# Performance work log

Hardware: AMD Instinct MI355X
Metric: run time of the kernel (lower is better)

Reference implementation:

```python
import jax, jax.numpy as jnp
import numpy as np

B, A, F = 8192, 8, 256      # batch, n_agents, per-agent obs feature dim
NA = 16                     # n_actions per agent
H1, H2 = 1024, 1024
OBS_D = A * F               # 2048 flattened obs dim
ACT_D = A * NA              # 128 joint action dim
IN_D = OBS_D + ACT_D        # 2176 MLP input dim


def setup_inputs() -> dict:
    key = jax.random.key(0)
    ks = jax.random.split(key, 8)
    s = 0.02
    return {
        "obs": jax.random.normal(ks[0], (B, A, F), dtype=jnp.float32),
        "all_actions": jax.random.uniform(ks[1], (B, ACT_D), dtype=jnp.float32),
        # per-agent stacked MLP params (agent axis first)
        "W1": jax.random.normal(ks[2], (A, IN_D, H1), dtype=jnp.float32) * s,
        "b1": jnp.zeros((A, H1), dtype=jnp.float32),
        "W2": jax.random.normal(ks[3], (A, H1, H2), dtype=jnp.float32) * s,
        "b2": jnp.zeros((A, H2), dtype=jnp.float32),
        "W3": jax.random.normal(ks[4], (A, H2, NA), dtype=jnp.float32) * s,
        "b3": jnp.zeros((A, NA), dtype=jnp.float32),
    }


def reference(obs, all_actions, W1, b1, W2, b2, W3, b3):
    b_s = obs.shape[0]
    obs_flat = obs.reshape(b_s, OBS_D)                      # [B, A*F]
    # mask[a, g] = 0 on agent a's own action block, 1 elsewhere
    mask = 1.0 - jnp.repeat(jnp.eye(A, dtype=obs.dtype), NA, axis=1)  # [A, A*NA]
    # split W1 into obs / action columns (equivalent to concat-then-dense)
    W1o = W1[:, :OBS_D, :]                                  # [A, OBS_D, H1]
    W1a = W1[:, OBS_D:, :]                                  # [A, ACT_D, H1]
    h1 = jax.nn.relu(
        jnp.einsum("bd,adh->bah", obs_flat, W1o)
        + jnp.einsum("bg,ag,agh->bah", all_actions, mask, W1a)
        + b1
    )                                                        # [B, A, H1]
    h2 = jax.nn.relu(jnp.einsum("bah,ahk->bak", h1, W2) + b2)  # [B, A, H2]
    out = jnp.einsum("bak,akn->ban", h2, W3) + b3              # [B, A, NA]
    return out.reshape(b_s, A * NA)
```

## Files before the change

kernel.cpp:

```cpp
#include <hip/hip_runtime.h>
#include <hip/hip_bf16.h>
#include <cstdint>
#include <cstddef>

typedef __bf16 bf16;
typedef __attribute__((ext_vector_type(8))) __bf16 bf16x8;
typedef __attribute__((ext_vector_type(4))) float f32x4;
typedef __attribute__((ext_vector_type(4))) int i32x4;
typedef __attribute__((address_space(3))) const bf16* lds_cp;

#define B_SZ  8192
#define NAGENT 8
#define NA_N  16
#define OBS_DD 2048
#define ACT_DD 128
#define IN_DD 2176
#define H1_D  1024
#define H2_D  1024

#define BM 256
#define BN 256
#define BK 64
#define GRID_M (B_SZ / BM)
#define GRID_N (1024 / BN)

__device__ __forceinline__ void gload16(const void* g, void* l) {
    __builtin_amdgcn_global_load_lds(
        (__attribute__((address_space(1))) void*)(g),
        (__attribute__((address_space(3))) void*)(l), 16, 0, 0);
}


__global__ void k_convert_x(const float* __restrict__ obs,
                            const float* __restrict__ act,
                            bf16* __restrict__ xb) {
    const int chunks = IN_DD / 8;
    int idx = blockIdx.x * blockDim.x + threadIdx.x;
    if (idx >= B_SZ * chunks) return;
    int b = idx / chunks;
    int c8 = idx - b * chunks;
    const float* src = (c8 < OBS_DD / 8)
        ? (obs + (size_t)b * OBS_DD + c8 * 8)
        : (act + (size_t)b * ACT_DD + (c8 - OBS_DD / 8) * 8);
    float4 v0 = ((const float4*)src)[0];
    float4 v1 = ((const float4*)src)[1];
    bf16x8 o;
    o[0] = (bf16)v0.x; o[1] = (bf16)v0.y; o[2] = (bf16)v0.z; o[3] = (bf16)v0.w;
    o[4] = (bf16)v1.x; o[5] = (bf16)v1.y; o[6] = (bf16)v1.z; o[7] = (bf16)v1.w;
    ((bf16x8*)(xb + (size_t)b * IN_DD))[c8] = o;
}

__global__ void k_transpose_w(const float* __restrict__ src, bf16* __restrict__ dst,
                              int K, int H, int maskStart) {
    __shared__ float tile[32][33];
    int a = blockIdx.z;
    int k0 = blockIdx.x * 32, h0 = blockIdx.y * 32;
    const float* s = src + (size_t)a * K * H;
    bf16* d = dst + (size_t)a * K * H;
    int tx = threadIdx.x, ty = threadIdx.y;
    #pragma unroll
    for (int i = 0; i < 32; i += 8) {
        int k = k0 + ty + i;
        float v = s[(size_t)k * H + h0 + tx];
        if (k >= maskStart) {
            int g = k - maskStart;
            if ((g >> 4) == a) v = 0.f;
        }
        tile[ty + i][tx] = v;
    }
    __syncthreads();
    #pragma unroll
    for (int i = 0; i < 32; i += 8) {
        d[(size_t)(h0 + ty + i) * K + k0 + tx] = (bf16)tile[tx][ty + i];
    }
}

__global__ void k_transpose_w3(const float* __restrict__ src, bf16* __restrict__ dst) {
    int idx = blockIdx.x * blockDim.x + threadIdx.x;
    if (idx >= NAGENT * NA_N * H2_D) return;
    int a = idx / (NA_N * H2_D);
    int n = (idx / H2_D) % NA_N;
    int k = idx % H2_D;
    dst[idx] = (bf16)src[(size_t)a * H2_D * NA_N + (size_t)k * NA_N + n];
}

__global__ void k_init_out(const float* __restrict__ b3, float* __restrict__ out) {
    int i = blockIdx.x * blockDim.x + threadIdx.x;
    if (i < B_SZ * NAGENT * NA_N) out[i] = b3[i & 127];
}

#define DSR4(d0, d1, d2, d3, addr, O0, O1, O2, O3)                      \
    asm volatile("ds_read_b128 %0, %4 offset:" #O0 "\n\t"               \
                 "ds_read_b128 %1, %4 offset:" #O1 "\n\t"               \
                 "ds_read_b128 %2, %4 offset:" #O2 "\n\t"               \
                 "ds_read_b128 %3, %4 offset:" #O3                      \
                 : "=&v"(d0), "=&v"(d1), "=&v"(d2), "=&v"(d3)           \
                 : "v"(addr))

#define BC(x) __builtin_bit_cast(bf16x8, x)

template<int FUSE>
__global__ __launch_bounds__(512, 1)
void k_gemm256(const bf16* __restrict__ Ain, size_t aStride, int lda,
               const bf16* __restrict__ Bw, const float* __restrict__ bias,
               bf16* __restrict__ Cout, size_t cStride, int K,
               int aOff, int gridZ,
               const bf16* __restrict__ W3Tp, float* __restrict__ outp) {
    extern __shared__ bf16 lds[];

    const int tid = threadIdx.x;
    const int w = tid >> 6;
    const int l = tid & 63;

    int flat = blockIdx.x + GRID_M * (blockIdx.y + GRID_N * blockIdx.z);
    int q8 = (GRID_M * GRID_N * gridZ) >> 3;
    int lin2 = (flat & 7) * q8 + (flat >> 3);
    const int mt = lin2 % GRID_M;
    int rest = lin2 / GRID_M;
    const int ntile = rest % GRID_N;
    const int az = rest / GRID_N;
    const int aw = az + aOff;

    const int rowBase = mt * BM;
    const int colBase = ntile * BN;
    const bf16* Aag = Ain + (size_t)az * aStride;
    const bf16* Bag = Bw + (size_t)aw * (size_t)1024 * K;

    const int wr = (w >> 2) * 128;
    const int wc = (w & 3) * 64;
    const int lr = l & 15;
    const int lq = l >> 4;

    const int rowA = (wr + lr) * BK;
    const int rowB = (wc + lr) * BK;
    const int ck0 = ((lq ^ (lr & 7)) * 8);
    const int ck1 = (((4 + lq) ^ (lr & 7)) * 8);

    const int sRow = w * 16 + (l >> 3);
    const int sCol = ((l & 7) ^ (l >> 3)) * 8;
    const bf16* pA0 = Aag + (size_t)(rowBase + sRow) * lda + sCol;
    const bf16* pA1 = Aag + (size_t)(rowBase + 128 + sRow) * lda + sCol;
    const bf16* pB0 = Bag + (size_t)(colBase + sRow) * K + sCol;
    const bf16* pB1 = Bag + (size_t)(colBase + 128 + sRow) * K + sCol;
    const size_t l8a = (size_t)8 * lda;
    const size_t l8b = (size_t)8 * K;

    const int nkt = K / BK;

#define STAGE_A(t1, half) do {                                              \
        const bf16* g_ = ((half) ? pA1 : pA0) + (t1) * BK;                  \
        bf16* d_ = &lds[(((t1) & 1) * 16384) + (half) * 8192 + w * 1024];   \
        gload16(g_, d_);                                                    \
        gload16(g_ + l8a, d_ + 512);                                        \
    } while (0)
#define STAGE_B(t2, half) do {                                              \
        const bf16* g_ = ((half) ? pB1 : pB0) + (t2) * BK;                  \
        bf16* d_ = &lds[32768 + (((t2) & 1) * 16384) + (half) * 8192 + w * 1024]; \
        gload16(g_, d_);                                                    \
        gload16(g_ + l8b, d_ + 512);                                        \
    } while (0)

    f32x4 acc[8][4] = {};
    i32x4 ra0, ra1, ra2, ra3;
    i32x4 rb0, rb1, rb2, rb3;
    i32x4 rc0, rc1, rc2, rc3;
    i32x4 rd0, rd1, rd2, rd3;
    i32x4 re0, re1, re2, re3;
    i32x4 rf0, rf1, rf2, rf3;

#define MFMA16(ACC0, A0, A1, A2, A3, B0, B1, B2, B3)                        \
    do {                                                                    \
        acc[ACC0+0][0] = __builtin_amdgcn_mfma_f32_16x16x32_bf16(BC(A0), BC(B0), acc[ACC0+0][0], 0, 0, 0); \
        acc[ACC0+1][0] = __builtin_amdgcn_mfma_f32_16x16x32_bf16(BC(A1), BC(B0), acc[ACC0+1][0], 0, 0, 0); \
        acc[ACC0+2][0] = __builtin_amdgcn_mfma_f32_16x16x32_bf16(BC(A2), BC(B0), acc[ACC0+2][0], 0, 0, 0); \
        acc[ACC0+3][0] = __builtin_amdgcn_mfma_f32_16x16x32_bf16(BC(A3), BC(B0), acc[ACC0+3][0], 0, 0, 0); \
        acc[ACC0+0][1] = __builtin_amdgcn_mfma_f32_16x16x32_bf16(BC(A0), BC(B1), acc[ACC0+0][1], 0, 0, 0); \
        acc[ACC0+1][1] = __builtin_amdgcn_mfma_f32_16x16x32_bf16(BC(A1), BC(B1), acc[ACC0+1][1], 0, 0, 0); \
        acc[ACC0+2][1] = __builtin_amdgcn_mfma_f32_16x16x32_bf16(BC(A2), BC(B1), acc[ACC0+2][1], 0, 0, 0); \
        acc[ACC0+3][1] = __builtin_amdgcn_mfma_f32_16x16x32_bf16(BC(A3), BC(B1), acc[ACC0+3][1], 0, 0, 0); \
        acc[ACC0+0][2] = __builtin_amdgcn_mfma_f32_16x16x32_bf16(BC(A0), BC(B2), acc[ACC0+0][2], 0, 0, 0); \
        acc[ACC0+1][2] = __builtin_amdgcn_mfma_f32_16x16x32_bf16(BC(A1), BC(B2), acc[ACC0+1][2], 0, 0, 0); \
        acc[ACC0+2][2] = __builtin_amdgcn_mfma_f32_16x16x32_bf16(BC(A2), BC(B2), acc[ACC0+2][2], 0, 0, 0); \
        acc[ACC0+3][2] = __builtin_amdgcn_mfma_f32_16x16x32_bf16(BC(A3), BC(B2), acc[ACC0+3][2], 0, 0, 0); \
        acc[ACC0+0][3] = __builtin_amdgcn_mfma_f32_16x16x32_bf16(BC(A0), BC(B3), acc[ACC0+0][3], 0, 0, 0); \
        acc[ACC0+1][3] = __builtin_amdgcn_mfma_f32_16x16x32_bf16(BC(A1), BC(B3), acc[ACC0+1][3], 0, 0, 0); \
        acc[ACC0+2][3] = __builtin_amdgcn_mfma_f32_16x16x32_bf16(BC(A2), BC(B3), acc[ACC0+2][3], 0, 0, 0); \
        acc[ACC0+3][3] = __builtin_amdgcn_mfma_f32_16x16x32_bf16(BC(A3), BC(B3), acc[ACC0+3][3], 0, 0, 0); \
    } while (0)

    STAGE_A(0, 0); STAGE_A(0, 1);
    STAGE_B(0, 0); STAGE_B(0, 1);
    asm volatile("s_waitcnt vmcnt(0)" ::: "memory");
    __builtin_amdgcn_s_barrier();

    for (int t = 0; t < nkt; ++t) {
        const int dbuf = (t & 1) * 16384;
        lds_cp adrA0 = (lds_cp)lds + (dbuf + rowA + ck0);
        lds_cp adrA1 = (lds_cp)lds + (dbuf + rowA + ck1);
        lds_cp adrB0 = (lds_cp)lds + (32768 + dbuf + rowB + ck0);
        lds_cp adrB1 = (lds_cp)lds + (32768 + dbuf + rowB + ck1);

        if (t + 1 < nkt) {
            STAGE_A(t + 1, 0); STAGE_A(t + 1, 1);
            STAGE_B(t + 1, 0); STAGE_B(t + 1, 1);
        }

        DSR4(ra0, ra1, ra2, ra3, adrA0, 0, 2048, 4096, 6144);
        DSR4(rb0, rb1, rb2, rb3, adrB0, 0, 2048, 4096, 6144);
        DSR4(rc0, rc1, rc2, rc3, adrA0, 8192, 10240, 12288, 14336);
        DSR4(rd0, rd1, rd2, rd3, adrB1, 0, 2048, 4096, 6144);

        asm volatile("s_waitcnt lgkmcnt(8)" ::: "memory");
        __builtin_amdgcn_sched_barrier(0);
        __builtin_amdgcn_s_setprio(1);
        MFMA16(0, ra0, ra1, ra2, ra3, rb0, rb1, rb2, rb3);
        __builtin_amdgcn_s_setprio(0);

        DSR4(re0, re1, re2, re3, adrA1, 0, 2048, 4096, 6144);
        asm volatile("s_waitcnt lgkmcnt(4)" ::: "memory");
        __builtin_amdgcn_sched_barrier(0);
        __builtin_amdgcn_s_setprio(1);
        MFMA16(4, rc0, rc1, rc2, rc3, rb0, rb1, rb2, rb3);
        __builtin_amdgcn_s_setprio(0);

        DSR4(rf0, rf1, rf2, rf3, adrA1, 8192, 10240, 12288, 14336);
        asm volatile("s_waitcnt lgkmcnt(4)" ::: "memory");
        __builtin_amdgcn_sched_barrier(0);
        __builtin_amdgcn_s_setprio(1);
        MFMA16(0, re0, re1, re2, re3, rd0, rd1, rd2, rd3);
        __builtin_amdgcn_s_setprio(0);

        asm volatile("s_waitcnt lgkmcnt(0)" ::: "memory");
        __builtin_amdgcn_sched_barrier(0);
        __builtin_amdgcn_s_setprio(1);
        MFMA16(4, rf0, rf1, rf2, rf3, rd0, rd1, rd2, rd3);
        __builtin_amdgcn_s_setprio(0);

        asm volatile("s_waitcnt vmcnt(0)" ::: "memory");
        __builtin_amdgcn_s_barrier();
    }
#undef STAGE_A
#undef STAGE_B
#undef MFMA16

    __syncthreads();
    const float* bAg = bias + (size_t)aw * 1024;
    float bb4[4];
    #pragma unroll
    for (int n = 0; n < 4; ++n) bb4[n] = bAg[colBase + wc + n * 16 + lr];
    #pragma unroll
    for (int m = 0; m < 8; ++m)
        #pragma unroll
        for (int n = 0; n < 4; ++n)
            #pragma unroll
            for (int r = 0; r < 4; ++r) {
                float v = acc[m][n][r] + bb4[n];
                v = fmaxf(v, 0.f);
                int row = wr + m * 16 + lq * 4 + r;
                int col = wc + n * 16 + lr;
                lds[row * 256 + ((((col >> 3) ^ (row & 7)) << 3) | (col & 7))] = (bf16)v;
            }
    __syncthreads();

    if constexpr (!FUSE) {
        bf16* Cg = Cout + (size_t)az * cStride + (size_t)rowBase * 1024 + colBase;
        const int er = tid >> 5;
        const int ec = tid & 31;
        #pragma unroll
        for (int i = 0; i < 16; ++i) {
            int row = i * 16 + er;
            int phys = ec ^ (row & 7);
            *(bf16x8*)&Cg[(size_t)row * 1024 + ec * 8] =
                *(const bf16x8*)&lds[row * 256 + phys * 8];
        }
    } else {
        const bf16* w3a = W3Tp + (size_t)aw * NA_N * H2_D;
        f32x4 oacc[2] = {};
        const int frow0 = w * 32;
        #pragma unroll
        for (int ks = 0; ks < 8; ++ks) {
            bf16x8 bfrag = *(const bf16x8*)&w3a[(size_t)lr * H2_D + colBase + ks * 32 + lq * 8];
            #pragma unroll
            for (int mm = 0; mm < 2; ++mm) {
                int row = frow0 + mm * 16 + lr;
                int lc = (ks * 4 + lq) ^ (row & 7);
                bf16x8 afrag = *(const bf16x8*)&lds[row * 256 + lc * 8];
                oacc[mm] = __builtin_amdgcn_mfma_f32_16x16x32_bf16(afrag, bfrag, oacc[mm], 0, 0, 0);
            }
        }
        #pragma unroll
        for (int mm = 0; mm < 2; ++mm)
            #pragma unroll
            for (int r = 0; r < 4; ++r)
                atomicAdd(&outp[(size_t)(rowBase + frow0 + mm * 16 + lq * 4 + r) * 128
                                + aw * NA_N + lr], oacc[mm][r]);
    }
}

extern "C" void kernel_launch(void* const* d_in, const int* in_sizes, int n_in,
                              void* d_out, int out_size, void* d_ws, size_t ws_size,
                              hipStream_t stream) {
    const float* obs = (const float*)d_in[0];
    const float* act = (const float*)d_in[1];
    const float* W1 = (const float*)d_in[2];
    const float* b1 = (const float*)d_in[3];
    const float* W2 = (const float*)d_in[4];
    const float* b2 = (const float*)d_in[5];
    const float* W3 = (const float*)d_in[6];
    const float* b3 = (const float*)d_in[7];
    float* out = (float*)d_out;

    const size_t SZ_XB  = (size_t)B_SZ * IN_DD * 2;
    const size_t SZ_W1T = (size_t)NAGENT * H1_D * IN_DD * 2;
    const size_t SZ_W2T = (size_t)NAGENT * H1_D * H2_D * 2;
    const size_t SZ_W3T = (size_t)NAGENT * NA_N * H2_D * 2;
    const size_t SZ_H1  = (size_t)B_SZ * H1_D * 2;
    const size_t SZ_FIX = SZ_XB + SZ_W1T + SZ_W2T + SZ_W3T;

    char* ws = (char*)d_ws;
    bf16* Xb  = (bf16*)ws;
    bf16* W1T = (bf16*)(ws + SZ_XB);
    bf16* W2T = (bf16*)(ws + SZ_XB + SZ_W1T);
    bf16* W3T = (bf16*)(ws + SZ_XB + SZ_W1T + SZ_W2T);
    char* hbase = ws + SZ_FIX;

    int G = 8;
    while (G > 1 && ws_size < SZ_FIX + (size_t)G * SZ_H1) G >>= 1;

    (void)hipFuncSetAttribute((const void*)k_gemm256<0>,
                              hipFuncAttributeMaxDynamicSharedMemorySize, 131072);
    (void)hipFuncSetAttribute((const void*)k_gemm256<1>,
                              hipFuncAttributeMaxDynamicSharedMemorySize, 131072);

    k_init_out<<<(B_SZ * 128 + 255) / 256, 256, 0, stream>>>(b3, out);

    {
        int n = B_SZ * (IN_DD / 8);
        k_convert_x<<<(n + 255) / 256, 256, 0, stream>>>(obs, act, Xb);
    }
    k_transpose_w<<<dim3(IN_DD / 32, H1_D / 32, NAGENT), dim3(32, 8), 0, stream>>>(
        W1, W1T, IN_DD, H1_D, OBS_DD);
    k_transpose_w<<<dim3(H1_D / 32, H2_D / 32, NAGENT), dim3(32, 8), 0, stream>>>(
        W2, W2T, H1_D, H2_D, 1 << 30);
    {
        int n = NAGENT * NA_N * H2_D;
        k_transpose_w3<<<(n + 255) / 256, 256, 0, stream>>>(W3, W3T);
    }

    const size_t agElems = (size_t)B_SZ * H1_D;
    bf16* h1 = (bf16*)hbase;

    for (int g0 = 0; g0 < NAGENT; g0 += G) {
        k_gemm256<0><<<dim3(GRID_M, GRID_N, G), 512, 131072, stream>>>(
            Xb, 0, IN_DD, W1T, b1, h1, agElems, IN_DD, g0, G, nullptr, nullptr);
        k_gemm256<1><<<dim3(GRID_M, GRID_N, G), 512, 131072, stream>>>(
            h1, agElems, H1_D, W2T, b2, nullptr, 0, H1_D, g0, G, W3T, out);
    }
    (void)in_sizes; (void)n_in; (void)out_size;
}
```

Measured before the change: 454.2 us.

## Shrink GEMM tiles to 128x128 with 4 waves and two blocks per CU

```diff
diff --git a/kernel.cpp b/kernel.cpp
--- a/kernel.cpp
+++ b/kernel.cpp
@@ -18,8 +18,8 @@
 #define H1_D  1024
 #define H2_D  1024
 
-#define BM 256
-#define BN 256
+#define BM 128
+#define BN 128
 #define BK 64
 #define GRID_M (B_SZ / BM)
 #define GRID_N (1024 / BN)
@@ -100,8 +100,8 @@
 #define BC(x) __builtin_bit_cast(bf16x8, x)
 
 template<int FUSE>
-__global__ __launch_bounds__(512, 1)
-void k_gemm256(const bf16* __restrict__ Ain, size_t aStride, int lda,
+__global__ __launch_bounds__(256, 2)
+void k_gemm128(const bf16* __restrict__ Ain, size_t aStride, int lda,
                const bf16* __restrict__ Bw, const float* __restrict__ bias,
                bf16* __restrict__ Cout, size_t cStride, int K,
                int aOff, int gridZ,
@@ -126,70 +126,69 @@
     const bf16* Aag = Ain + (size_t)az * aStride;
     const bf16* Bag = Bw + (size_t)aw * (size_t)1024 * K;
 
-    const int wr = (w >> 2) * 128;
-    const int wc = (w & 3) * 64;
+    const int wr = (w >> 1) * 64;
+    const int wc = (w & 1) * 64;
     const int lr = l & 15;
     const int lq = l >> 4;
 
-    const int rowA = (wr + lr) * BK;
-    const int rowB = (wc + lr) * BK;
+    const int rowA = (wr + lr) * 64;
+    const int rowB = 8192 + (wc + lr) * 64;
     const int ck0 = ((lq ^ (lr & 7)) * 8);
     const int ck1 = (((4 + lq) ^ (lr & 7)) * 8);
 
-    const int sRow = w * 16 + (l >> 3);
+    const int sRow = w * 32 + (l >> 3);
     const int sCol = ((l & 7) ^ (l >> 3)) * 8;
-    const bf16* pA0 = Aag + (size_t)(rowBase + sRow) * lda + sCol;
-    const bf16* pA1 = Aag + (size_t)(rowBase + 128 + sRow) * lda + sCol;
-    const bf16* pB0 = Bag + (size_t)(colBase + sRow) * K + sCol;
-    const bf16* pB1 = Bag + (size_t)(colBase + 128 + sRow) * K + sCol;
+    const bf16* pA = Aag + (size_t)(rowBase + sRow) * lda + sCol;
+    const bf16* pB = Bag + (size_t)(colBase + sRow) * K + sCol;
     const size_t l8a = (size_t)8 * lda;
     const size_t l8b = (size_t)8 * K;
 
     const int nkt = K / BK;
 
-#define STAGE_A(t1, half) do {                                              \
-        const bf16* g_ = ((half) ? pA1 : pA0) + (t1) * BK;                  \
-        bf16* d_ = &lds[(((t1) & 1) * 16384) + (half) * 8192 + w * 1024];   \
+#define STAGE_A(t1) do {                                                    \
+        const bf16* g_ = pA + (t1) * BK;                                    \
+        bf16* d_ = &lds[(((t1) & 1) * 16384) + w * 2048];                   \
         gload16(g_, d_);                                                    \
         gload16(g_ + l8a, d_ + 512);                                        \
+        gload16(g_ + 2 * l8a, d_ + 1024);                                   \
+        gload16(g_ + 3 * l8a, d_ + 1536);                                   \
     } while (0)
-#define STAGE_B(t2, half) do {                                              \
-        const bf16* g_ = ((half) ? pB1 : pB0) + (t2) * BK;                  \
-        bf16* d_ = &lds[32768 + (((t2) & 1) * 16384) + (half) * 8192 + w * 1024]; \
+#define STAGE_B(t1) do {                                                    \
+        const bf16* g_ = pB + (t1) * BK;                                    \
+        bf16* d_ = &lds[(((t1) & 1) * 16384) + 8192 + w * 2048];            \
         gload16(g_, d_);                                                    \
         gload16(g_ + l8b, d_ + 512);                                        \
+        gload16(g_ + 2 * l8b, d_ + 1024);                                   \
+        gload16(g_ + 3 * l8b, d_ + 1536);                                   \
     } while (0)
 
-    f32x4 acc[8][4] = {};
+    f32x4 acc[4][4] = {};
     i32x4 ra0, ra1, ra2, ra3;
     i32x4 rb0, rb1, rb2, rb3;
     i32x4 rc0, rc1, rc2, rc3;
     i32x4 rd0, rd1, rd2, rd3;
-    i32x4 re0, re1, re2, re3;
-    i32x4 rf0, rf1, rf2, rf3;
-
-#define MFMA16(ACC0, A0, A1, A2, A3, B0, B1, B2, B3)                        \
+
+#define MFMA16(A0, A1, A2, A3, B0, B1, B2, B3)                              \
     do {                                                                    \
-        acc[ACC0+0][0] = __builtin_amdgcn_mfma_f32_16x16x32_bf16(BC(A0), BC(B0), acc[ACC0+0][0], 0, 0, 0); \
-        acc[ACC0+1][0] = __builtin_amdgcn_mfma_f32_16x16x32_bf16(BC(A1), BC(B0), acc[ACC0+1][0], 0, 0, 0); \
-        acc[ACC0+2][0] = __builtin_amdgcn_mfma_f32_16x16x32_bf16(BC(A2), BC(B0), acc[ACC0+2][0], 0, 0, 0); \
-        acc[ACC0+3][0] = __builtin_amdgcn_mfma_f32_16x16x32_bf16(BC(A3), BC(B0), acc[ACC0+3][0], 0, 0, 0); \
-        acc[ACC0+0][1] = __builtin_amdgcn_mfma_f32_16x16x32_bf16(BC(A0), BC(B1), acc[ACC0+0][1], 0, 0, 0); \
-        acc[ACC0+1][1] = __builtin_amdgcn_mfma_f32_16x16x32_bf16(BC(A1), BC(B1), acc[ACC0+1][1], 0, 0, 0); \
-        acc[ACC0+2][1] = __builtin_amdgcn_mfma_f32_16x16x32_bf16(BC(A2), BC(B1), acc[ACC0+2][1], 0, 0, 0); \
-        acc[ACC0+3][1] = __builtin_amdgcn_mfma_f32_16x16x32_bf16(BC(A3), BC(B1), acc[ACC0+3][1], 0, 0, 0); \
-        acc[ACC0+0][2] = __builtin_amdgcn_mfma_f32_16x16x32_bf16(BC(A0), BC(B2), acc[ACC0+0][2], 0, 0, 0); \
-        acc[ACC0+1][2] = __builtin_amdgcn_mfma_f32_16x16x32_bf16(BC(A1), BC(B2), acc[ACC0+1][2], 0, 0, 0); \
-        acc[ACC0+2][2] = __builtin_amdgcn_mfma_f32_16x16x32_bf16(BC(A2), BC(B2), acc[ACC0+2][2], 0, 0, 0); \
-        acc[ACC0+3][2] = __builtin_amdgcn_mfma_f32_16x16x32_bf16(BC(A3), BC(B2), acc[ACC0+3][2], 0, 0, 0); \
-        acc[ACC0+0][3] = __builtin_amdgcn_mfma_f32_16x16x32_bf16(BC(A0), BC(B3), acc[ACC0+0][3], 0, 0, 0); \
-        acc[ACC0+1][3] = __builtin_amdgcn_mfma_f32_16x16x32_bf16(BC(A1), BC(B3), acc[ACC0+1][3], 0, 0, 0); \
-        acc[ACC0+2][3] = __builtin_amdgcn_mfma_f32_16x16x32_bf16(BC(A2), BC(B3), acc[ACC0+2][3], 0, 0, 0); \
-        acc[ACC0+3][3] = __builtin_amdgcn_mfma_f32_16x16x32_bf16(BC(A3), BC(B3), acc[ACC0+3][3], 0, 0, 0); \
+        acc[0][0] = __builtin_amdgcn_mfma_f32_16x16x32_bf16(BC(A0), BC(B0), acc[0][0], 0, 0, 0); \
+        acc[1][0] = __builtin_amdgcn_mfma_f32_16x16x32_bf16(BC(A1), BC(B0), acc[1][0], 0, 0, 0); \
+        acc[2][0] = __builtin_amdgcn_mfma_f32_16x16x32_bf16(BC(A2), BC(B0), acc[2][0], 0, 0, 0); \
+        acc[3][0] = __builtin_amdgcn_mfma_f32_16x16x32_bf16(BC(A3), BC(B0), acc[3][0], 0, 0, 0); \
+        acc[0][1] = __builtin_amdgcn_mfma_f32_16x16x32_bf16(BC(A0), BC(B1), acc[0][1], 0, 0, 0); \
+        acc[1][1] = __builtin_amdgcn_mfma_f32_16x16x32_bf16(BC(A1), BC(B1), acc[1][1], 0, 0, 0); \
+        acc[2][1] = __builtin_amdgcn_mfma_f32_16x16x32_bf16(BC(A2), BC(B1), acc[2][1], 0, 0, 0); \
+        acc[3][1] = __builtin_amdgcn_mfma_f32_16x16x32_bf16(BC(A3), BC(B1), acc[3][1], 0, 0, 0); \
+        acc[0][2] = __builtin_amdgcn_mfma_f32_16x16x32_bf16(BC(A0), BC(B2), acc[0][2], 0, 0, 0); \
+        acc[1][2] = __builtin_amdgcn_mfma_f32_16x16x32_bf16(BC(A1), BC(B2), acc[1][2], 0, 0, 0); \
+        acc[2][2] = __builtin_amdgcn_mfma_f32_16x16x32_bf16(BC(A2), BC(B2), acc[2][2], 0, 0, 0); \
+        acc[3][2] = __builtin_amdgcn_mfma_f32_16x16x32_bf16(BC(A3), BC(B2), acc[3][2], 0, 0, 0); \
+        acc[0][3] = __builtin_amdgcn_mfma_f32_16x16x32_bf16(BC(A0), BC(B3), acc[0][3], 0, 0, 0); \
+        acc[1][3] = __builtin_amdgcn_mfma_f32_16x16x32_bf16(BC(A1), BC(B3), acc[1][3], 0, 0, 0); \
+        acc[2][3] = __builtin_amdgcn_mfma_f32_16x16x32_bf16(BC(A2), BC(B3), acc[2][3], 0, 0, 0); \
+        acc[3][3] = __builtin_amdgcn_mfma_f32_16x16x32_bf16(BC(A3), BC(B3), acc[3][3], 0, 0, 0); \
     } while (0)
 
-    STAGE_A(0, 0); STAGE_A(0, 1);
-    STAGE_B(0, 0); STAGE_B(0, 1);
+    STAGE_A(0); STAGE_B(0);
     asm volatile("s_waitcnt vmcnt(0)" ::: "memory");
     __builtin_amdgcn_s_barrier();
 
@@ -197,43 +196,26 @@
         const int dbuf = (t & 1) * 16384;
         lds_cp adrA0 = (lds_cp)lds + (dbuf + rowA + ck0);
         lds_cp adrA1 = (lds_cp)lds + (dbuf + rowA + ck1);
-        lds_cp adrB0 = (lds_cp)lds + (32768 + dbuf + rowB + ck0);
-        lds_cp adrB1 = (lds_cp)lds + (32768 + dbuf + rowB + ck1);
-
-        if (t + 1 < nkt) {
-            STAGE_A(t + 1, 0); STAGE_A(t + 1, 1);
-            STAGE_B(t + 1, 0); STAGE_B(t + 1, 1);
-        }
+        lds_cp adrB0 = (lds_cp)lds + (dbuf + rowB + ck0);
+        lds_cp adrB1 = (lds_cp)lds + (dbuf + rowB + ck1);
+
+        if (t + 1 < nkt) { STAGE_A(t + 1); STAGE_B(t + 1); }
 
         DSR4(ra0, ra1, ra2, ra3, adrA0, 0, 2048, 4096, 6144);
         DSR4(rb0, rb1, rb2, rb3, adrB0, 0, 2048, 4096, 6144);
-        DSR4(rc0, rc1, rc2, rc3, adrA0, 8192, 10240, 12288, 14336);
+        DSR4(rc0, rc1, rc2, rc3, adrA1, 0, 2048, 4096, 6144);
         DSR4(rd0, rd1, rd2, rd3, adrB1, 0, 2048, 4096, 6144);
 
         asm volatile("s_waitcnt lgkmcnt(8)" ::: "memory");
         __builtin_amdgcn_sched_barrier(0);
         __builtin_amdgcn_s_setprio(1);
-        MFMA16(0, ra0, ra1, ra2, ra3, rb0, rb1, rb2, rb3);
-        __builtin_amdgcn_s_setprio(0);
-
-        DSR4(re0, re1, re2, re3, adrA1, 0, 2048, 4096, 6144);
-        asm volatile("s_waitcnt lgkmcnt(4)" ::: "memory");
-        __builtin_amdgcn_sched_barrier(0);
-        __builtin_amdgcn_s_setprio(1);
-        MFMA16(4, rc0, rc1, rc2, rc3, rb0, rb1, rb2, rb3);
-        __builtin_amdgcn_s_setprio(0);
-
-        DSR4(rf0, rf1, rf2, rf3, adrA1, 8192, 10240, 12288, 14336);
-        asm volatile("s_waitcnt lgkmcnt(4)" ::: "memory");
-        __builtin_amdgcn_sched_barrier(0);
-        __builtin_amdgcn_s_setprio(1);
-        MFMA16(0, re0, re1, re2, re3, rd0, rd1, rd2, rd3);
+        MFMA16(ra0, ra1, ra2, ra3, rb0, rb1, rb2, rb3);
         __builtin_amdgcn_s_setprio(0);
 
         asm volatile("s_waitcnt lgkmcnt(0)" ::: "memory");
         __builtin_amdgcn_sched_barrier(0);
         __builtin_amdgcn_s_setprio(1);
-        MFMA16(4, rf0, rf1, rf2, rf3, rd0, rd1, rd2, rd3);
+        MFMA16(rc0, rc1, rc2, rc3, rd0, rd1, rd2, rd3);
         __builtin_amdgcn_s_setprio(0);
 
         asm volatile("s_waitcnt vmcnt(0)" ::: "memory");
@@ -249,7 +231,7 @@
     #pragma unroll
     for (int n = 0; n < 4; ++n) bb4[n] = bAg[colBase + wc + n * 16 + lr];
     #pragma unroll
-    for (int m = 0; m < 8; ++m)
+    for (int m = 0; m < 4; ++m)
         #pragma unroll
         for (int n = 0; n < 4; ++n)
             #pragma unroll
@@ -258,33 +240,33 @@
                 v = fmaxf(v, 0.f);
                 int row = wr + m * 16 + lq * 4 + r;
                 int col = wc + n * 16 + lr;
-                lds[row * 256 + ((((col >> 3) ^ (row & 7)) << 3) | (col & 7))] = (bf16)v;
+                lds[row * 128 + ((((col >> 3) ^ (row & 7)) << 3) | (col & 7))] = (bf16)v;
             }
     __syncthreads();
 
     if constexpr (!FUSE) {
         bf16* Cg = Cout + (size_t)az * cStride + (size_t)rowBase * 1024 + colBase;
-        const int er = tid >> 5;
-        const int ec = tid & 31;
+        const int er = tid >> 4;
+        const int ec = tid & 15;
         #pragma unroll
-        for (int i = 0; i < 16; ++i) {
+        for (int i = 0; i < 8; ++i) {
             int row = i * 16 + er;
             int phys = ec ^ (row & 7);
             *(bf16x8*)&Cg[(size_t)row * 1024 + ec * 8] =
-                *(const bf16x8*)&lds[row * 256 + phys * 8];
+                *(const bf16x8*)&lds[row * 128 + phys * 8];
         }
     } else {
         const bf16* w3a = W3Tp + (size_t)aw * NA_N * H2_D;
         f32x4 oacc[2] = {};
         const int frow0 = w * 32;
         #pragma unroll
-        for (int ks = 0; ks < 8; ++ks) {
+        for (int ks = 0; ks < 4; ++ks) {
             bf16x8 bfrag = *(const bf16x8*)&w3a[(size_t)lr * H2_D + colBase + ks * 32 + lq * 8];
             #pragma unroll
             for (int mm = 0; mm < 2; ++mm) {
                 int row = frow0 + mm * 16 + lr;
                 int lc = (ks * 4 + lq) ^ (row & 7);
-                bf16x8 afrag = *(const bf16x8*)&lds[row * 256 + lc * 8];
+                bf16x8 afrag = *(const bf16x8*)&lds[row * 128 + lc * 8];
                 oacc[mm] = __builtin_amdgcn_mfma_f32_16x16x32_bf16(afrag, bfrag, oacc[mm], 0, 0, 0);
             }
         }
@@ -327,10 +309,10 @@
     int G = 8;
     while (G > 1 && ws_size < SZ_FIX + (size_t)G * SZ_H1) G >>= 1;
 
-    (void)hipFuncSetAttribute((const void*)k_gemm256<0>,
-                              hipFuncAttributeMaxDynamicSharedMemorySize, 131072);
-    (void)hipFuncSetAttribute((const void*)k_gemm256<1>,
-                              hipFuncAttributeMaxDynamicSharedMemorySize, 131072);
+    (void)hipFuncSetAttribute((const void*)k_gemm128<0>,
+                              hipFuncAttributeMaxDynamicSharedMemorySize, 65536);
+    (void)hipFuncSetAttribute((const void*)k_gemm128<1>,
+                              hipFuncAttributeMaxDynamicSharedMemorySize, 65536);
 
     k_init_out<<<(B_SZ * 128 + 255) / 256, 256, 0, stream>>>(b3, out);
 
@@ -351,9 +333,9 @@
     bf16* h1 = (bf16*)hbase;
 
     for (int g0 = 0; g0 < NAGENT; g0 += G) {
-        k_gemm256<0><<<dim3(GRID_M, GRID_N, G), 512, 131072, stream>>>(
+        k_gemm128<0><<<dim3(GRID_M, GRID_N, G), 256, 65536, stream>>>(
             Xb, 0, IN_DD, W1T, b1, h1, agElems, IN_DD, g0, G, nullptr, nullptr);
-        k_gemm256<1><<<dim3(GRID_M, GRID_N, G), 512, 131072, stream>>>(
+        k_gemm128<1><<<dim3(GRID_M, GRID_N, G), 256, 65536, stream>>>(
             h1, agElems, H1_D, W2T, b2, nullptr, 0, H1_D, g0, G, W3T, out);
     }
     (void)in_sizes; (void)n_in; (void)out_size;
```

Measured after the change: 561.3 us. 1.24x slower.
